# Kernel tuning notes

Hardware: AMD Instinct MI355X
Metric: run time of the kernel (lower is better)

Reference implementation:

```python
import jax, jax.numpy as jnp
import numpy as np

EMBED = 512
HEADS = 8
HEAD_DIM = EMBED // HEADS
SCALE_BASE = 512
NEG = -1e9


def xpos_apply(x, offset, downscale):
    # x: [(b h), L, d]
    L, d = x.shape[1], x.shape[2]
    min_pos = -(L + offset) // 2
    max_pos = L + offset + min_pos
    base = (jnp.arange(0, d, 2, dtype=jnp.float32) + 0.4 * d) / (1.4 * d)      # [d/2]
    power = jnp.arange(min_pos, max_pos, dtype=jnp.float32) / SCALE_BASE        # [L']
    scale = base[None, :] ** power[:, None]                                     # [L', d/2]
    half = d // 2
    inv_freq = 1.0 / (10000.0 ** (jnp.arange(half, dtype=jnp.float32) / half))
    sinusoid = jnp.arange(scale.shape[0], dtype=jnp.float32)[:, None] * inv_freq[None, :]
    sin, cos = jnp.sin(sinusoid), jnp.cos(sinusoid)
    # keep last L rows (no-op when offset == 0)
    scale, sin, cos = scale[-L:], sin[-L:], cos[-L:]
    if downscale:
        scale = 1.0 / scale
    sin2 = jnp.repeat(sin * scale, 2, axis=-1)   # duplicate_interleave -> [L, d]
    cos2 = jnp.repeat(cos * scale, 2, axis=-1)
    x1, x2 = x[..., ::2], x[..., 1::2]
    rot = jnp.stack([-x2, x1], axis=-1).reshape(x.shape)  # rotate_every_two
    return x * cos2[None] + rot * sin2[None]


def split_heads(x, b, L):
    # 'b l (h d) -> (b h) l d'
    return x.reshape(b, L, HEADS, HEAD_DIM).transpose(0, 2, 1, 3).reshape(b * HEADS, L, HEAD_DIM)


def setup_inputs() -> dict:
    key = jax.random.key(0)
    ks = jax.random.split(key, 12)
    b, L = 4, 2048
    inp = {
        'query': jax.random.normal(ks[0], (b, L, EMBED), jnp.float32),
        'key': jax.random.normal(ks[1], (b, L, EMBED), jnp.float32),
        'value': jax.random.normal(ks[2], (b, L, EMBED), jnp.float32),
        'key_padding_mask': jnp.zeros((b, L), jnp.bool_),
        'attn_mask': jnp.where(jnp.tril(jnp.ones((L, L), jnp.bool_)), 0.0, NEG).astype(jnp.float32),
    }
    s = 1.0 / np.sqrt(EMBED)
    inp['Wq'] = jax.random.normal(ks[3], (EMBED, EMBED), jnp.float32) * s
    inp['bq'] = jnp.zeros((EMBED,), jnp.float32)
    inp['Wk'] = jax.random.normal(ks[4], (EMBED, EMBED), jnp.float32) * s
    inp['bk'] = jnp.zeros((EMBED,), jnp.float32)
    inp['Wv'] = jax.random.normal(ks[5], (EMBED, EMBED), jnp.float32) * s
    inp['bv'] = jnp.zeros((EMBED,), jnp.float32)
    inp['Wo'] = jax.random.normal(ks[6], (EMBED, EMBED), jnp.float32) * s
    inp['bo'] = jnp.zeros((EMBED,), jnp.float32)
    return inp


def reference(query, key, value, key_padding_mask, attn_mask, Wq, bq, Wk, bk, Wv, bv, Wo, bo):
    b, L, _ = query.shape
    q = split_heads(query @ Wq.T + bq, b, L)
    k = split_heads(key @ Wk.T + bk, b, L)
    v = split_heads(value @ Wv.T + bv, b, L)
    k = xpos_apply(k, 0, True)
    q = xpos_apply(q, 0, False)
    q = q * (HEAD_DIM ** -0.5)
    aw = jnp.einsum('btd,bsd->bts', q, k)                 # [(b h), t, s]
    aw = jnp.nan_to_num(aw) + attn_mask[None]
    aw = aw.reshape(b, HEADS, L, L)
    aw = jnp.where(key_padding_mask[:, None, None, :], jnp.finfo(aw.dtype).min, aw)
    aw = aw.reshape(b * HEADS, L, L)
    probs = jax.nn.softmax(aw.astype(jnp.float32), axis=-1).astype(aw.dtype)
    attn = jnp.einsum('bts,bsd->btd', probs, v)           # [(b h), t, d]
    attn = attn.reshape(b, HEADS, L, HEAD_DIM).transpose(0, 2, 1, 3).reshape(b, L, EMBED)
    return attn @ Wo.T + bo
```

## Files before the change

kernel.cpp:

```cpp
#include <hip/hip_runtime.h>
#include <hip/hip_bf16.h>

typedef __bf16 bf16x2 __attribute__((ext_vector_type(2)));
typedef __bf16 bf16x4 __attribute__((ext_vector_type(4)));
typedef __bf16 bf16x8 __attribute__((ext_vector_type(8)));
typedef float  f32x4  __attribute__((ext_vector_type(4)));

#define SEQ    2048
#define EMB    512
#define NHEAD  8
#define HD     64
#define NBATCH 4
#define MROWS  (NBATCH*SEQ)
#define QSCALE 0.18033688011112042f
#define INV2PI 0.15915494309189535f
#define TWOPI  6.28318530717958648f
#define NEGFREQ (-0.41524101186092028f)

__device__ __forceinline__ f32x4 mfma16(bf16x8 a, bf16x8 b, f32x4 c) {
  return __builtin_amdgcn_mfma_f32_16x16x32_bf16(a, b, c, 0, 0, 0);
}

typedef __attribute__((address_space(1))) const void gv_t;
typedef __attribute__((address_space(3))) void lv_t;
__device__ __forceinline__ void async16(const void* g, void* l) {
  __builtin_amdgcn_global_load_lds((gv_t*)g, (lv_t*)l, 16, 0, 0);
}

__global__ __launch_bounds__(256) void conv_kernel(const float* __restrict__ q,
                                                   const float* __restrict__ k,
                                                   const float* __restrict__ v,
                                                   __bf16* __restrict__ Qf,
                                                   __bf16* __restrict__ Kf,
                                                   __bf16* __restrict__ Vf) {
  const int z = blockIdx.y;
  const float* src = (z == 0) ? q : (z == 1) ? k : v;
  __bf16* dst = (z == 0) ? Qf : (z == 1) ? Kf : Vf;
  const size_t i8 = ((size_t)blockIdx.x * 256 + threadIdx.x) * 8;
  const float4 fa = ((const float4*)(src + i8))[0];
  const float4 fb = ((const float4*)(src + i8))[1];
  bf16x8 h = { (__bf16)fa.x, (__bf16)fa.y, (__bf16)fa.z, (__bf16)fa.w,
               (__bf16)fb.x, (__bf16)fb.y, (__bf16)fb.z, (__bf16)fb.w };
  *(bf16x8*)(dst + i8) = h;
}

__global__ __launch_bounds__(256) void convw_kernel(const float* __restrict__ wq,
                                                    const float* __restrict__ wk,
                                                    const float* __restrict__ wv,
                                                    const float* __restrict__ wo,
                                                    __bf16* __restrict__ Wb) {
  const int z = blockIdx.x >> 7;
  const float* src = (z == 0) ? wq : (z == 1) ? wk : (z == 2) ? wv : wo;
  __bf16* dst = Wb + (size_t)z * (EMB * EMB);
  const size_t i8 = ((size_t)(blockIdx.x & 127) * 256 + threadIdx.x) * 8;
  const float4 fa = ((const float4*)(src + i8))[0];
  const float4 fb = ((const float4*)(src + i8))[1];
  bf16x8 h = { (__bf16)fa.x, (__bf16)fa.y, (__bf16)fa.z, (__bf16)fa.w,
               (__bf16)fb.x, (__bf16)fb.y, (__bf16)fb.z, (__bf16)fb.w };
  *(bf16x8*)(dst + i8) = h;
}

__device__ __forceinline__ void gemm_main(const __bf16* __restrict__ A,
                                          const __bf16* __restrict__ W,
                                          __bf16* As, __bf16* Bs,
                                          f32x4 (&acc)[4][4], int m0, int n0) {
  const int tid = threadIdx.x;
  const int wid = tid >> 6, lane = tid & 63;
  const int quad = lane >> 4, l16 = lane & 15;
  const int l7 = l16 & 7;
  const int srow = lane >> 3;
  const int sxor = ((lane & 7) ^ srow) * 8;
  const int wm = (wid >> 1) * 64, wn = (wid & 1) * 64;

  #pragma unroll
  for (int i = 0; i < 4; ++i)
    #pragma unroll
    for (int j = 0; j < 4; ++j) acc[i][j] = (f32x4)(0.0f);

  for (int k0 = 0; k0 < 512; k0 += 64) {
    __syncthreads();
    #pragma unroll
    for (int ii = 0; ii < 4; ++ii) {
      const int r8 = wid * 32 + ii * 8;
      async16(A + (size_t)(m0 + r8 + srow) * 512 + k0 + sxor, &As[r8 * 64]);
      async16(W + (size_t)(n0 + r8 + srow) * 512 + k0 + sxor, &Bs[r8 * 64]);
    }
    __syncthreads();
    #pragma unroll
    for (int ks = 0; ks < 2; ++ks) {
      bf16x8 af[4], bfr[4];
      #pragma unroll
      for (int i = 0; i < 4; ++i)
        af[i] = *(const bf16x8*)&As[(wm + i * 16 + l16) * 64 +
                                    (((quad + ks * 4) ^ l7) * 8)];
      #pragma unroll
      for (int j = 0; j < 4; ++j)
        bfr[j] = *(const bf16x8*)&Bs[(wn + j * 16 + l16) * 64 +
                                     (((quad + ks * 4) ^ l7) * 8)];
      #pragma unroll
      for (int i = 0; i < 4; ++i)
        #pragma unroll
        for (int j = 0; j < 4; ++j)
          acc[i][j] = mfma16(af[i], bfr[j], acc[i][j]);
    }
  }
}

__global__ __launch_bounds__(256) void gemm_proj_kernel(
    const __bf16* __restrict__ Qf, const __bf16* __restrict__ Kf, const __bf16* __restrict__ Vf,
    const __bf16* __restrict__ Wb,
    const float* __restrict__ bq, const float* __restrict__ bk, const float* __restrict__ bv,
    __bf16* __restrict__ Qx, __bf16* __restrict__ Kx, __bf16* __restrict__ Vt) {
  __shared__ __align__(16) char smem[34816];
  __bf16* As = (__bf16*)smem;
  __bf16* Bs = (__bf16*)(smem + 16384);
  __bf16* T  = (__bf16*)smem;

  const int z = blockIdx.z;
  const __bf16* A = (z == 0) ? Qf : (z == 1) ? Kf : Vf;
  const __bf16* W = Wb + (size_t)z * (EMB * EMB);
  const float* bias = (z == 0) ? bq : (z == 1) ? bk : bv;
  const int m0 = blockIdx.y * 128, n0 = blockIdx.x * 128;

  f32x4 acc[4][4];
  gemm_main(A, W, As, Bs, acc, m0, n0);

  const int tid = threadIdx.x;
  const int wid = tid >> 6, lane = tid & 63;
  const int quad = lane >> 4, l16 = lane & 15;
  const int wm = (wid >> 1) * 64, wn = (wid & 1) * 64;

  __syncthreads();

  if (z == 2) {
    #pragma unroll
    for (int j = 0; j < 4; ++j) {
      const float bval = bias[n0 + wn + j * 16 + l16];
      #pragma unroll
      for (int i = 0; i < 4; ++i) {
        bf16x4 p = { (__bf16)(acc[i][j][0] + bval), (__bf16)(acc[i][j][1] + bval),
                     (__bf16)(acc[i][j][2] + bval), (__bf16)(acc[i][j][3] + bval) };
        *(bf16x4*)&T[(wn + j * 16 + l16) * 136 + wm + i * 16 + quad * 4] = p;
      }
    }
    __syncthreads();
    const int nrow = tid >> 1, mh = (tid & 1) << 6;
    bf16x8 vv[8];
    #pragma unroll
    for (int u = 0; u < 8; ++u) vv[u] = *(const bf16x8*)&T[nrow * 136 + mh + u * 8];
    const int n = n0 + nrow, h = n >> 6, d = n & 63;
    const int bb = m0 >> 11, lb2 = (m0 & 2047) + mh;
    __bf16* dst = Vt + ((size_t)(bb * 8 + h) * 64 + d) * 2048 + lb2;
    #pragma unroll
    for (int u = 0; u < 8; ++u) *(bf16x8*)(dst + u * 8) = vv[u];
  } else {
    #pragma unroll
    for (int j = 0; j < 4; ++j) {
      const float bval = bias[n0 + wn + j * 16 + l16];
      #pragma unroll
      for (int i = 0; i < 4; ++i)
        #pragma unroll
        for (int r = 0; r < 4; ++r)
          T[(wm + i * 16 + quad * 4 + r) * 136 + wn + j * 16 + l16] =
              (__bf16)(acc[i][j][r] + bval);
    }
    __syncthreads();
    const int lrow = tid >> 1, half = tid & 1;
    const int gm = m0 + lrow, l = gm & 2047, bb = gm >> 11;
    const int h = (n0 >> 6) + half;
    bf16x8 vv[8];
    #pragma unroll
    for (int u = 0; u < 8; ++u)
      vv[u] = *(const bf16x8*)&T[lrow * 136 + half * 64 + u * 8];
    bf16x8 ov[8];
    const float lf = (float)l;
    const float pw = (lf - 1024.0f) * (1.0f / 512.0f);
    const float qs = (z == 0) ? QSCALE : 1.0f;
    #pragma unroll
    for (int i = 0; i < 32; ++i) {
      const float x1 = (float)vv[i >> 2][(2 * i) & 7];
      const float x2 = (float)vv[i >> 2][(2 * i + 1) & 7];
      const float lb = __log2f((2.0f * i + 25.6f) * (1.0f / 89.6f));
      const float e  = (z == 0) ? (pw * lb) : (-pw * lb);
      const float sc = __builtin_amdgcn_exp2f(e) * qs;
      const float ang = lf * __builtin_amdgcn_exp2f((float)i * NEGFREQ);
      float rev = ang * INV2PI;
      rev -= floorf(rev);
      const float ar = rev * TWOPI;
      const float sn = __sinf(ar) * sc;
      const float cs = __cosf(ar) * sc;
      ov[i >> 2][(2 * i) & 7]     = (__bf16)(x1 * cs - x2 * sn);
      ov[i >> 2][(2 * i + 1) & 7] = (__bf16)(x2 * cs + x1 * sn);
    }
    __bf16* dst = ((z == 0) ? Qx : Kx) + ((size_t)(bb * 8 + h) * 2048 + l) * 64;
    #pragma unroll
    for (int u = 0; u < 8; ++u) *(bf16x8*)(dst + u * 8) = ov[u];
  }
}

__global__ __launch_bounds__(256) void gemm_out_kernel(
    const __bf16* __restrict__ A, const __bf16* __restrict__ W,
    const float* __restrict__ bias, float* __restrict__ C) {
  __shared__ __align__(16) char smem[34816];
  __bf16* As = (__bf16*)smem;
  __bf16* Bs = (__bf16*)(smem + 16384);
  const int m0 = blockIdx.y * 128, n0 = blockIdx.x * 128;
  f32x4 acc[4][4];
  gemm_main(A, W, As, Bs, acc, m0, n0);
  const int tid = threadIdx.x;
  const int wid = tid >> 6, lane = tid & 63;
  const int quad = lane >> 4, l16 = lane & 15;
  const int wm = (wid >> 1) * 64, wn = (wid & 1) * 64;
  #pragma unroll
  for (int j = 0; j < 4; ++j) {
    const int n = n0 + wn + j * 16 + l16;
    const float bval = bias[n];
    #pragma unroll
    for (int i = 0; i < 4; ++i)
      #pragma unroll
      for (int r = 0; r < 4; ++r)
        C[(size_t)(m0 + wm + i * 16 + quad * 4 + r) * 512 + n] = acc[i][j][r] + bval;
  }
}

__global__ __launch_bounds__(256) void flash_kernel(const __bf16* __restrict__ Qx,
                                                    const __bf16* __restrict__ Kx,
                                                    const __bf16* __restrict__ Vt,
                                                    const unsigned char* __restrict__ kpm,
                                                    __bf16* __restrict__ Oa) {
  __shared__ __align__(16) __bf16 Qs[64 * HD];
  __shared__ __align__(16) __bf16 Ks[64 * HD];
  __shared__ __align__(16) __bf16 Vs[64 * HD];
  __shared__ __align__(16) __bf16 Ps[4][16 * 72];

  const int tid = threadIdx.x;
  const int wid = tid >> 6;
  const int lane = tid & 63;
  const int quad = lane >> 4;
  const int l16 = lane & 15;
  const int srow = lane >> 3;
  const int sxor = ((lane & 7) ^ srow) * 8;
  const int l7 = l16 & 7;
  const int bh = blockIdx.x;
  const int b = bh >> 3;
  const int qb = 31 - (int)blockIdx.y;
  const int q0 = qb * 64;

  const __bf16* Qbase = Qx + (size_t)bh * (SEQ * HD);
  const __bf16* Kbase = Kx + (size_t)bh * (SEQ * HD);
  const __bf16* Vbase = Vt + (size_t)bh * (HD * SEQ);
  __bf16* Pw = &Ps[wid][0];

  #pragma unroll
  for (int ii = 0; ii < 2; ++ii) {
    const int r0 = wid * 16 + ii * 8;
    async16(Qbase + (size_t)(q0 + r0 + srow) * HD + sxor, &Qs[r0 * HD]);
  }
  __syncthreads();
  const bf16x8 qf0 = *(const bf16x8*)&Qs[(wid * 16 + l16) * HD + ((quad ^ l7) * 8)];
  const bf16x8 qf1 = *(const bf16x8*)&Qs[(wid * 16 + l16) * HD + (((quad + 4) ^ l7) * 8)];

  f32x4 o0 = (f32x4)(0.0f), o1 = (f32x4)(0.0f), o2 = (f32x4)(0.0f), o3 = (f32x4)(0.0f);
  float m_run = -1e30f, l_run = 0.0f;
  const int myq = q0 + wid * 16 + l16;

  for (int kv0 = 0; kv0 < q0 + 64; kv0 += 64) {
    __syncthreads();
    #pragma unroll
    for (int ii = 0; ii < 2; ++ii) {
      const int r0 = wid * 16 + ii * 8;
      async16(Kbase + (size_t)(kv0 + r0 + srow) * HD + sxor, &Ks[r0 * HD]);
      async16(Vbase + (size_t)(r0 + srow) * SEQ + kv0 + sxor, &Vs[r0 * HD]);
    }
    __syncthreads();

    f32x4 s[4];
    #pragma unroll
    for (int nb = 0; nb < 4; ++nb) s[nb] = (f32x4)(0.0f);
    #pragma unroll
    for (int nb = 0; nb < 4; ++nb) {
      const bf16x8 kf = *(const bf16x8*)&Ks[(nb * 16 + l16) * HD + ((quad ^ l7) * 8)];
      s[nb] = mfma16(kf, qf0, s[nb]);
    }
    #pragma unroll
    for (int nb = 0; nb < 4; ++nb) {
      const bf16x8 kf = *(const bf16x8*)&Ks[(nb * 16 + l16) * HD + (((quad + 4) ^ l7) * 8)];
      s[nb] = mfma16(kf, qf1, s[nb]);
    }

    if (kv0 + 63 > q0 + wid * 16) {
      #pragma unroll
      for (int nb = 0; nb < 4; ++nb)
        #pragma unroll
        for (int r = 0; r < 4; ++r)
          if (kv0 + nb * 16 + quad * 4 + r > myq) s[nb][r] = -1e30f;
    }
    {
      const unsigned char* kp0 = kpm + b * SEQ + kv0;
      #pragma unroll
      for (int nb = 0; nb < 4; ++nb) {
        const unsigned pk = *(const unsigned*)(kp0 + nb * 16 + quad * 4);
        if (pk) {
          if (pk & 0x000000FFu) s[nb][0] = -1e30f;
          if (pk & 0x0000FF00u) s[nb][1] = -1e30f;
          if (pk & 0x00FF0000u) s[nb][2] = -1e30f;
          if (pk & 0xFF000000u) s[nb][3] = -1e30f;
        }
      }
    }

    float mx = s[0][0];
    #pragma unroll
    for (int nb = 0; nb < 4; ++nb)
      #pragma unroll
      for (int r = 0; r < 4; ++r) mx = fmaxf(mx, s[nb][r]);
    mx = fmaxf(mx, __shfl_xor(mx, 16));
    mx = fmaxf(mx, __shfl_xor(mx, 32));
    const float m_new = fmaxf(m_run, mx);
    const float alpha = __builtin_amdgcn_exp2f(m_run - m_new);
    m_run = m_new;
    float ssum = 0.0f;
    #pragma unroll
    for (int nb = 0; nb < 4; ++nb) {
      #pragma unroll
      for (int r = 0; r < 4; ++r) {
        const float p = __builtin_amdgcn_exp2f(s[nb][r] - m_new);
        s[nb][r] = p;
        ssum += p;
      }
    }
    ssum += __shfl_xor(ssum, 16);
    ssum += __shfl_xor(ssum, 32);
    l_run = l_run * alpha + ssum;

    #pragma unroll
    for (int nb = 0; nb < 4; ++nb) {
      bf16x4 p4 = { (__bf16)s[nb][0], (__bf16)s[nb][1],
                    (__bf16)s[nb][2], (__bf16)s[nb][3] };
      *(bf16x4*)&Pw[l16 * 72 + nb * 16 + quad * 4] = p4;
    }
    o0 *= alpha; o1 *= alpha; o2 *= alpha; o3 *= alpha;

    #pragma unroll
    for (int ks = 0; ks < 2; ++ks) {
      const bf16x8 pf = *(const bf16x8*)&Pw[l16 * 72 + ks * 32 + quad * 8];
      const int bx = ((quad + ks * 4) ^ l7) * 8;
      o0 = mfma16(*(const bf16x8*)&Vs[( 0 + l16) * HD + bx], pf, o0);
      o1 = mfma16(*(const bf16x8*)&Vs[(16 + l16) * HD + bx], pf, o1);
      o2 = mfma16(*(const bf16x8*)&Vs[(32 + l16) * HD + bx], pf, o2);
      o3 = mfma16(*(const bf16x8*)&Vs[(48 + l16) * HD + bx], pf, o3);
    }
  }

  const float inv_l = 1.0f / l_run;
  {
    bf16x4 t0 = { (__bf16)(o0[0] * inv_l), (__bf16)(o0[1] * inv_l),
                  (__bf16)(o0[2] * inv_l), (__bf16)(o0[3] * inv_l) };
    bf16x4 t1 = { (__bf16)(o1[0] * inv_l), (__bf16)(o1[1] * inv_l),
                  (__bf16)(o1[2] * inv_l), (__bf16)(o1[3] * inv_l) };
    bf16x4 t2 = { (__bf16)(o2[0] * inv_l), (__bf16)(o2[1] * inv_l),
                  (__bf16)(o2[2] * inv_l), (__bf16)(o2[3] * inv_l) };
    bf16x4 t3 = { (__bf16)(o3[0] * inv_l), (__bf16)(o3[1] * inv_l),
                  (__bf16)(o3[2] * inv_l), (__bf16)(o3[3] * inv_l) };
    *(bf16x4*)&Pw[l16 * 72 +  0 + quad * 4] = t0;
    *(bf16x4*)&Pw[l16 * 72 + 16 + quad * 4] = t1;
    *(bf16x4*)&Pw[l16 * 72 + 32 + quad * 4] = t2;
    *(bf16x4*)&Pw[l16 * 72 + 48 + quad * 4] = t3;
  }
  const int h = bh & 7;
  #pragma unroll
  for (int ii = 0; ii < 2; ++ii) {
    const int qr = ii * 8 + (lane >> 3);
    const bf16x8 ovv = *(const bf16x8*)&Pw[qr * 72 + (lane & 7) * 8];
    *(bf16x8*)(Oa + (((size_t)b * SEQ + q0 + wid * 16 + qr) * NHEAD + h) * HD +
               (lane & 7) * 8) = ovv;
  }
}

extern "C" void kernel_launch(void* const* d_in, const int* in_sizes, int n_in,
                              void* d_out, int out_size, void* d_ws, size_t ws_size,
                              hipStream_t stream) {
  (void)in_sizes; (void)n_in; (void)out_size; (void)ws_size;
  const float* query = (const float*)d_in[0];
  const float* key   = (const float*)d_in[1];
  const float* value = (const float*)d_in[2];
  const unsigned char* kpm = (const unsigned char*)d_in[3];
  const float* Wq = (const float*)d_in[5];
  const float* bq = (const float*)d_in[6];
  const float* Wk = (const float*)d_in[7];
  const float* bk = (const float*)d_in[8];
  const float* Wv = (const float*)d_in[9];
  const float* bv = (const float*)d_in[10];
  const float* Wo = (const float*)d_in[11];
  const float* bo = (const float*)d_in[12];
  float* out = (float*)d_out;

  char* ws = (char*)d_ws;
  const size_t SZ = (size_t)MROWS * EMB * 2;
  __bf16* Qf = (__bf16*)(ws);
  __bf16* Kf = (__bf16*)(ws + SZ);
  __bf16* Vf = (__bf16*)(ws + 2 * SZ);
  __bf16* Qx = (__bf16*)(ws + 3 * SZ);
  __bf16* Kx = (__bf16*)(ws + 4 * SZ);
  __bf16* Vt = (__bf16*)(ws + 5 * SZ);
  __bf16* Wb = (__bf16*)(ws + 6 * SZ);
  __bf16* Oa = Qf;

  conv_kernel<<<dim3(2048, 3), dim3(256), 0, stream>>>(query, key, value, Qf, Kf, Vf);
  convw_kernel<<<dim3(512), dim3(256), 0, stream>>>(Wq, Wk, Wv, Wo, Wb);
  gemm_proj_kernel<<<dim3(4, 64, 3), dim3(256), 0, stream>>>(
      Qf, Kf, Vf, Wb, bq, bk, bv, Qx, Kx, Vt);
  flash_kernel<<<dim3(32, 32), dim3(256), 0, stream>>>(Qx, Kx, Vt, kpm, Oa);
  gemm_out_kernel<<<dim3(4, 64), dim3(256), 0, stream>>>(
      Oa, Wb + (size_t)3 * EMB * EMB, bo, out);
}
```

Measured before the change: 219.0 us.

## Double-buffer K/V tiles in flash attention and reuse Q smem for P

The flash attention loop now double-buffers K and V in shared memory, prefetching the next tile asynchronously while the current one is computed, and needs only one barrier per iteration instead of two. The per-wave P staging buffer now lives in the Q shared region (already consumed into registers), using an XOR-swizzled layout instead of padding. The online-softmax rescale is skipped when no lane's max increased, the max and sum reductions are tree-shaped, and s_setprio is raised around the MFMA blocks. This is meant to hide global-load latency and cut barrier and softmax overhead, at the cost of more shared memory and a subtle ordering dependency: the next-tile prefetch is issued with no wait visible before its tile is consumed, which relies on async-copy completion semantics not shown here.

```diff
diff --git a/kernel.cpp b/kernel.cpp
--- a/kernel.cpp
+++ b/kernel.cpp
@@ -228,19 +228,18 @@
                                                     const __bf16* __restrict__ Vt,
                                                     const unsigned char* __restrict__ kpm,
                                                     __bf16* __restrict__ Oa) {
+  __shared__ __align__(16) __bf16 Ks[2][64 * HD];
+  __shared__ __align__(16) __bf16 Vs[2][64 * HD];
   __shared__ __align__(16) __bf16 Qs[64 * HD];
-  __shared__ __align__(16) __bf16 Ks[64 * HD];
-  __shared__ __align__(16) __bf16 Vs[64 * HD];
-  __shared__ __align__(16) __bf16 Ps[4][16 * 72];
 
   const int tid = threadIdx.x;
   const int wid = tid >> 6;
   const int lane = tid & 63;
   const int quad = lane >> 4;
   const int l16 = lane & 15;
+  const int l7 = l16 & 7;
   const int srow = lane >> 3;
   const int sxor = ((lane & 7) ^ srow) * 8;
-  const int l7 = l16 & 7;
   const int bh = blockIdx.x;
   const int b = bh >> 3;
   const int qb = 31 - (int)blockIdx.y;
@@ -249,12 +248,14 @@
   const __bf16* Qbase = Qx + (size_t)bh * (SEQ * HD);
   const __bf16* Kbase = Kx + (size_t)bh * (SEQ * HD);
   const __bf16* Vbase = Vt + (size_t)bh * (HD * SEQ);
-  __bf16* Pw = &Ps[wid][0];
+  __bf16* Pw = Qs + wid * 1024;
 
   #pragma unroll
   for (int ii = 0; ii < 2; ++ii) {
     const int r0 = wid * 16 + ii * 8;
     async16(Qbase + (size_t)(q0 + r0 + srow) * HD + sxor, &Qs[r0 * HD]);
+    async16(Kbase + (size_t)(r0 + srow) * HD + sxor, &Ks[0][r0 * HD]);
+    async16(Vbase + (size_t)(r0 + srow) * SEQ + sxor, &Vs[0][r0 * HD]);
   }
   __syncthreads();
   const bf16x8 qf0 = *(const bf16x8*)&Qs[(wid * 16 + l16) * HD + ((quad ^ l7) * 8)];
@@ -263,30 +264,44 @@
   f32x4 o0 = (f32x4)(0.0f), o1 = (f32x4)(0.0f), o2 = (f32x4)(0.0f), o3 = (f32x4)(0.0f);
   float m_run = -1e30f, l_run = 0.0f;
   const int myq = q0 + wid * 16 + l16;
-
-  for (int kv0 = 0; kv0 < q0 + 64; kv0 += 64) {
-    __syncthreads();
-    #pragma unroll
-    for (int ii = 0; ii < 2; ++ii) {
-      const int r0 = wid * 16 + ii * 8;
-      async16(Kbase + (size_t)(kv0 + r0 + srow) * HD + sxor, &Ks[r0 * HD]);
-      async16(Vbase + (size_t)(r0 + srow) * SEQ + kv0 + sxor, &Vs[r0 * HD]);
-    }
-    __syncthreads();
+  const int niter = qb + 1;
+
+  for (int it = 0; it < niter; ++it) {
+    const int kv0 = it << 6;
+    const int cur = it & 1;
+    const __bf16* Kc = &Ks[cur][0];
+    const __bf16* Vc = &Vs[cur][0];
+
+    if (it + 1 < niter) {
+      const int kn = kv0 + 64;
+      #pragma unroll
+      for (int ii = 0; ii < 2; ++ii) {
+        const int r0 = wid * 16 + ii * 8;
+        async16(Kbase + (size_t)(kn + r0 + srow) * HD + sxor, &Ks[cur ^ 1][r0 * HD]);
+        async16(Vbase + (size_t)(r0 + srow) * SEQ + kn + sxor, &Vs[cur ^ 1][r0 * HD]);
+      }
+    }
+    const unsigned char* kp0 = kpm + b * SEQ + kv0;
+    unsigned pk[4];
+    #pragma unroll
+    for (int nb = 0; nb < 4; ++nb)
+      pk[nb] = *(const unsigned*)(kp0 + nb * 16 + quad * 4);
 
     f32x4 s[4];
     #pragma unroll
     for (int nb = 0; nb < 4; ++nb) s[nb] = (f32x4)(0.0f);
+    __builtin_amdgcn_s_setprio(1);
     #pragma unroll
     for (int nb = 0; nb < 4; ++nb) {
-      const bf16x8 kf = *(const bf16x8*)&Ks[(nb * 16 + l16) * HD + ((quad ^ l7) * 8)];
+      const bf16x8 kf = *(const bf16x8*)&Kc[(nb * 16 + l16) * HD + ((quad ^ l7) * 8)];
       s[nb] = mfma16(kf, qf0, s[nb]);
     }
     #pragma unroll
     for (int nb = 0; nb < 4; ++nb) {
-      const bf16x8 kf = *(const bf16x8*)&Ks[(nb * 16 + l16) * HD + (((quad + 4) ^ l7) * 8)];
+      const bf16x8 kf = *(const bf16x8*)&Kc[(nb * 16 + l16) * HD + (((quad + 4) ^ l7) * 8)];
       s[nb] = mfma16(kf, qf1, s[nb]);
     }
+    __builtin_amdgcn_s_setprio(0);
 
     if (kv0 + 63 > q0 + wid * 16) {
       #pragma unroll
@@ -295,61 +310,71 @@
         for (int r = 0; r < 4; ++r)
           if (kv0 + nb * 16 + quad * 4 + r > myq) s[nb][r] = -1e30f;
     }
+    #pragma unroll
+    for (int nb = 0; nb < 4; ++nb) {
+      if (pk[nb]) {
+        if (pk[nb] & 0x000000FFu) s[nb][0] = -1e30f;
+        if (pk[nb] & 0x0000FF00u) s[nb][1] = -1e30f;
+        if (pk[nb] & 0x00FF0000u) s[nb][2] = -1e30f;
+        if (pk[nb] & 0xFF000000u) s[nb][3] = -1e30f;
+      }
+    }
+
+    float mx;
     {
-      const unsigned char* kp0 = kpm + b * SEQ + kv0;
-      #pragma unroll
-      for (int nb = 0; nb < 4; ++nb) {
-        const unsigned pk = *(const unsigned*)(kp0 + nb * 16 + quad * 4);
-        if (pk) {
-          if (pk & 0x000000FFu) s[nb][0] = -1e30f;
-          if (pk & 0x0000FF00u) s[nb][1] = -1e30f;
-          if (pk & 0x00FF0000u) s[nb][2] = -1e30f;
-          if (pk & 0xFF000000u) s[nb][3] = -1e30f;
-        }
-      }
-    }
-
-    float mx = s[0][0];
-    #pragma unroll
-    for (int nb = 0; nb < 4; ++nb)
-      #pragma unroll
-      for (int r = 0; r < 4; ++r) mx = fmaxf(mx, s[nb][r]);
+      f32x4 u0, u1;
+      #pragma unroll
+      for (int r = 0; r < 4; ++r) u0[r] = fmaxf(s[0][r], s[1][r]);
+      #pragma unroll
+      for (int r = 0; r < 4; ++r) u1[r] = fmaxf(s[2][r], s[3][r]);
+      #pragma unroll
+      for (int r = 0; r < 4; ++r) u0[r] = fmaxf(u0[r], u1[r]);
+      mx = fmaxf(fmaxf(u0[0], u0[1]), fmaxf(u0[2], u0[3]));
+    }
     mx = fmaxf(mx, __shfl_xor(mx, 16));
     mx = fmaxf(mx, __shfl_xor(mx, 32));
-    const float m_new = fmaxf(m_run, mx);
-    const float alpha = __builtin_amdgcn_exp2f(m_run - m_new);
-    m_run = m_new;
-    float ssum = 0.0f;
-    #pragma unroll
-    for (int nb = 0; nb < 4; ++nb) {
-      #pragma unroll
-      for (int r = 0; r < 4; ++r) {
-        const float p = __builtin_amdgcn_exp2f(s[nb][r] - m_new);
-        s[nb][r] = p;
-        ssum += p;
-      }
-    }
-    ssum += __shfl_xor(ssum, 16);
-    ssum += __shfl_xor(ssum, 32);
-    l_run = l_run * alpha + ssum;
+    if (__any(mx > m_run)) {
+      const float m_new = fmaxf(m_run, mx);
+      const float alpha = __builtin_amdgcn_exp2f(m_run - m_new);
+      o0 *= alpha; o1 *= alpha; o2 *= alpha; o3 *= alpha;
+      l_run *= alpha;
+      m_run = m_new;
+    }
+    #pragma unroll
+    for (int nb = 0; nb < 4; ++nb)
+      #pragma unroll
+      for (int r = 0; r < 4; ++r)
+        s[nb][r] = __builtin_amdgcn_exp2f(s[nb][r] - m_run);
+    {
+      f32x4 v01 = s[0] + s[1];
+      f32x4 v23 = s[2] + s[3];
+      f32x4 vt = v01 + v23;
+      float ssum = (vt[0] + vt[1]) + (vt[2] + vt[3]);
+      ssum += __shfl_xor(ssum, 16);
+      ssum += __shfl_xor(ssum, 32);
+      l_run += ssum;
+    }
 
     #pragma unroll
     for (int nb = 0; nb < 4; ++nb) {
       bf16x4 p4 = { (__bf16)s[nb][0], (__bf16)s[nb][1],
                     (__bf16)s[nb][2], (__bf16)s[nb][3] };
-      *(bf16x4*)&Pw[l16 * 72 + nb * 16 + quad * 4] = p4;
-    }
-    o0 *= alpha; o1 *= alpha; o2 *= alpha; o3 *= alpha;
-
+      *(bf16x4*)&Pw[l16 * 64 + (((nb * 2 + (quad >> 1)) ^ l7) << 3) + (quad & 1) * 4] = p4;
+    }
+
+    __builtin_amdgcn_s_setprio(1);
     #pragma unroll
     for (int ks = 0; ks < 2; ++ks) {
-      const bf16x8 pf = *(const bf16x8*)&Pw[l16 * 72 + ks * 32 + quad * 8];
+      const bf16x8 pf = *(const bf16x8*)&Pw[l16 * 64 + (((ks * 4 + quad) ^ l7) << 3)];
       const int bx = ((quad + ks * 4) ^ l7) * 8;
-      o0 = mfma16(*(const bf16x8*)&Vs[( 0 + l16) * HD + bx], pf, o0);
-      o1 = mfma16(*(const bf16x8*)&Vs[(16 + l16) * HD + bx], pf, o1);
-      o2 = mfma16(*(const bf16x8*)&Vs[(32 + l16) * HD + bx], pf, o2);
-      o3 = mfma16(*(const bf16x8*)&Vs[(48 + l16) * HD + bx], pf, o3);
-    }
+      o0 = mfma16(*(const bf16x8*)&Vc[( 0 + l16) * HD + bx], pf, o0);
+      o1 = mfma16(*(const bf16x8*)&Vc[(16 + l16) * HD + bx], pf, o1);
+      o2 = mfma16(*(const bf16x8*)&Vc[(32 + l16) * HD + bx], pf, o2);
+      o3 = mfma16(*(const bf16x8*)&Vc[(48 + l16) * HD + bx], pf, o3);
+    }
+    __builtin_amdgcn_s_setprio(0);
+
+    if (it + 1 < niter) __syncthreads();
   }
 
   const float inv_l = 1.0f / l_run;
@@ -362,16 +387,16 @@
                   (__bf16)(o2[2] * inv_l), (__bf16)(o2[3] * inv_l) };
     bf16x4 t3 = { (__bf16)(o3[0] * inv_l), (__bf16)(o3[1] * inv_l),
                   (__bf16)(o3[2] * inv_l), (__bf16)(o3[3] * inv_l) };
-    *(bf16x4*)&Pw[l16 * 72 +  0 + quad * 4] = t0;
-    *(bf16x4*)&Pw[l16 * 72 + 16 + quad * 4] = t1;
-    *(bf16x4*)&Pw[l16 * 72 + 32 + quad * 4] = t2;
-    *(bf16x4*)&Pw[l16 * 72 + 48 + quad * 4] = t3;
+    *(bf16x4*)&Pw[l16 * 64 + (((0 + (quad >> 1)) ^ l7) << 3) + (quad & 1) * 4] = t0;
+    *(bf16x4*)&Pw[l16 * 64 + (((2 + (quad >> 1)) ^ l7) << 3) + (quad & 1) * 4] = t1;
+    *(bf16x4*)&Pw[l16 * 64 + (((4 + (quad >> 1)) ^ l7) << 3) + (quad & 1) * 4] = t2;
+    *(bf16x4*)&Pw[l16 * 64 + (((6 + (quad >> 1)) ^ l7) << 3) + (quad & 1) * 4] = t3;
   }
   const int h = bh & 7;
   #pragma unroll
   for (int ii = 0; ii < 2; ++ii) {
     const int qr = ii * 8 + (lane >> 3);
-    const bf16x8 ovv = *(const bf16x8*)&Pw[qr * 72 + (lane & 7) * 8];
+    const bf16x8 ovv = *(const bf16x8*)&Pw[qr * 64 + (((lane & 7) ^ (qr & 7)) << 3)];
     *(bf16x8*)(Oa + (((size_t)b * SEQ + q0 + wid * 16 + qr) * NHEAD + h) * HD +
                (lane & 7) * 8) = ovv;
   }
```

Result: faster. 213.2 us (-2.6%).
